# Kernel optimization log

Measured on AMD Instinct MI355X. Metric: run time of the kernel, lower is better.

The kernel has to match this reference:

```python
import jax, jax.numpy as jnp
import numpy as np

N_BINS = 50
FEATURE_ID = 0
EPS = 1e-7  # keras backend epsilon used by binary_crossentropy clipping


def setup_inputs() -> dict:
    key = jax.random.key(0)
    k1, k2 = jax.random.split(key)
    inputs = jax.random.normal(k1, (8_000_000, 4), dtype=jnp.float32)
    targets = jax.random.randint(k2, (8_000_000,), 0, 2, dtype=jnp.int32)
    return {"inputs": inputs, "targets": targets}


def _cut_forward(inputs, targets):
    # x: selected feature column, y: binary labels
    x = inputs[:, FEATURE_ID]
    y = targets
    N = x.shape[0]
    n_f = jnp.float32(N)

    x_min = jnp.min(x)
    x_max = jnp.max(x)
    E = N_BINS + 1
    edges = jnp.linspace(x_min, x_max, E)

    # Sort events once; prefix-sum of signal labels gives exact class counts
    # below/above any threshold (equivalent to the per-bin compare+count loop,
    # including the original's inclusive [lower, upper] double-counting of edges).
    order = jnp.argsort(x)
    xs = x[order]
    ys = (y[order] == 1).astype(jnp.float32)
    cs = jnp.concatenate([jnp.zeros((1,), jnp.float32), jnp.cumsum(ys)])  # [N+1]
    Ns = cs[-1]
    Nb = n_f - Ns

    r = jnp.searchsorted(xs, edges, side='right')  # count(x <= e)
    l = jnp.searchsorted(xs, edges, side='left')   # count(x <  e)
    ns_le = cs[r]
    ns_lt = cs[l]
    nb_le = r.astype(jnp.float32) - ns_le
    nb_lt = l.astype(jnp.float32) - ns_lt

    # hist[i] = count(lower[i] <= v <= upper[i]) per class
    hist0 = nb_le[1:] - nb_lt[:-1]  # background, [N_BINS]
    hist1 = ns_le[1:] - ns_lt[:-1]  # signal

    # candidate bin edges: sign-flip boundaries of hist0>hist1 with non-empty bins
    gt0 = hist0 > hist1
    cand0 = jnp.logical_xor(gt0[:-1], gt0[1:]) & (hist0[:-1] > 0)
    gt1 = hist1 > hist0
    cand1 = jnp.logical_xor(gt1[:-1], gt1[1:]) & (hist1[:-1] > 0)
    mask = jnp.zeros((E,), bool).at[1:N_BINS].set(cand0 | cand1)
    cnt = jnp.sum(mask)
    # original appends x_max when exactly one candidate survives
    mask = mask.at[-1].set(mask[-1] | (cnt == 1))

    # clipped BCE on hard 0/1 predictions reduces to a weighted error count:
    # correct sample -> -log(1-eps), wrong sample -> -log(eps)
    a = -jnp.log1p(jnp.float32(-EPS))
    b = -jnp.log(jnp.float32(EPS))

    def bce(correct):
        return ((n_f - correct) * b + correct * a) / n_f

    # per-edge losses for single-threshold cases
    c0 = ns_le + (Nb - nb_le)          # case 0: pred = (x <= c)
    c1 = (Ns - ns_lt) + nb_lt          # case 1: pred = (x >= c)
    # per-pair losses (i = lower cut, j = upper cut)
    c2 = (ns_le[None, :] - ns_lt[:, None]) + Nb - (nb_le[None, :] - nb_lt[:, None])
    c3 = ns_le[:, None] + (Ns - ns_lt[None, :]) + (nb_le[None, :] - nb_lt[:, None])

    L = jnp.stack([
        jnp.broadcast_to(bce(c0)[:, None], (E, E)),
        jnp.broadcast_to(bce(c1)[:, None], (E, E)),
        bce(c2),
        bce(c3),
    ])  # [4, E, E]
    per_pair_min = jnp.min(L, axis=0)
    per_pair_case = jnp.argmin(L, axis=0)

    idx = jnp.arange(E)
    valid = mask[:, None] & mask[None, :] & (idx[:, None] < idx[None, :])
    flat = jnp.argmin(jnp.where(valid, per_pair_min, jnp.inf))
    i = flat // E
    j = flat % E
    lower = edges[i]
    upper = edges[j]
    case = per_pair_case[i, j]

    pred0 = x <= lower
    pred1 = x >= lower
    pred2 = pred1 & (x <= upper)
    pred3 = pred0 | (x >= upper)
    y_pred = jnp.where(case == 0, pred0,
             jnp.where(case == 1, pred1,
             jnp.where(case == 2, pred2, pred3)))
    return y_pred


def reference(inputs, targets):
    return _cut_forward(inputs, targets).astype(jnp.int32)
```

## Files before the change

### kernel.cpp

```cpp
#include <hip/hip_runtime.h>
#include <math.h>
#include <stdint.h>

#define N_BINS 50
#define EDGE_N 51
#define HIST_N 52
#define NBLK 2048
#define NTHR 256

typedef unsigned int u32;
typedef unsigned short u16;
typedef unsigned char u8;


__device__ __forceinline__ float edge_at(int e, float xmin, float xmax) {
  if (e >= N_BINS) return xmax;
  float step = __fdiv_rn((float)e, (float)N_BINS);
  float omst = __fsub_rn(1.0f, step);
  return __fadd_rn(__fmul_rn(xmin, omst), __fmul_rn(xmax, step));
}

__device__ __forceinline__ float bce_f(int c, float n_f, float aC, float bC) {
  float cf = (float)c;
  float t = __fadd_rn(__fmul_rn(__fsub_rn(n_f, cf), bC), __fmul_rn(cf, aC));
  return __fdiv_rn(t, n_f);
}

__device__ __forceinline__ void get_ab(float& aC, float& bC) {
  const double epsd = (double)1e-7f;
  aC = (float)(-log1p(-epsd));
  bC = (float)(-log(epsd));
}

__device__ __forceinline__ void global_minmax(const float* __restrict__ bmin,
                                              const float* __restrict__ bmax,
                                              float* s_red, float* s_mm) {
  const int tid = threadIdx.x;
  float m = INFINITY, M = -INFINITY;
  for (int i = tid; i < NBLK; i += NTHR) { m = fminf(m, bmin[i]); M = fmaxf(M, bmax[i]); }
  for (int off = 32; off; off >>= 1) {
    m = fminf(m, __shfl_down(m, off));
    M = fmaxf(M, __shfl_down(M, off));
  }
  int wid = tid >> 6;
  if ((tid & 63) == 0) { s_red[wid] = m; s_red[4 + wid] = M; }
  __syncthreads();
  if (tid == 0) {
    float mm = s_red[0], MM = s_red[4];
    for (int w = 1; w < NTHR / 64; ++w) { mm = fminf(mm, s_red[w]); MM = fmaxf(MM, s_red[4 + w]); }
    s_mm[0] = mm;
    s_mm[1] = MM;
  }
  __syncthreads();
}

template <int COMPACT>
__global__ void k_minmax(const float4* __restrict__ in4, int n,
                         float* __restrict__ bmin, float* __restrict__ bmax,
                         int* __restrict__ histU, int* __restrict__ histE,
                         float* __restrict__ xc) {
  const int tid = threadIdx.x, bid = blockIdx.x;
  const int gid = bid * NTHR + tid;
  const int stride = NBLK * NTHR;
  const int nv = n >> 2;
  const int base = nv << 2;
  float4* __restrict__ xc4 = (float4*)xc;
  if (bid == 0) {
    for (int i = tid; i < 2 * HIST_N; i += NTHR) histU[i] = 0;
    for (int i = tid; i < 2 * EDGE_N; i += NTHR) histE[i] = 0;
  }
  float vmin = INFINITY, vmax = -INFINITY;
  for (int iv = gid; iv < nv; iv += stride) {
    float4 a = in4[4 * iv + 0];
    float4 b = in4[4 * iv + 1];
    float4 c = in4[4 * iv + 2];
    float4 d = in4[4 * iv + 3];
    vmin = fminf(fminf(vmin, fminf(a.x, b.x)), fminf(c.x, d.x));
    vmax = fmaxf(fmaxf(vmax, fmaxf(a.x, b.x)), fmaxf(c.x, d.x));
    if (COMPACT) xc4[iv] = make_float4(a.x, b.x, c.x, d.x);
  }
  if (bid == 0 && tid < (n - base)) {
    float x = in4[base + tid].x;
    vmin = fminf(vmin, x);
    vmax = fmaxf(vmax, x);
    if (COMPACT) xc[base + tid] = x;
  }
  for (int off = 32; off; off >>= 1) {
    vmin = fminf(vmin, __shfl_down(vmin, off));
    vmax = fmaxf(vmax, __shfl_down(vmax, off));
  }
  __shared__ float s_red[8];
  int wid = tid >> 6;
  if ((tid & 63) == 0) { s_red[wid] = vmin; s_red[4 + wid] = vmax; }
  __syncthreads();
  if (tid == 0) {
    float m = s_red[0], M = s_red[4];
    for (int w = 1; w < NTHR / 64; ++w) { m = fminf(m, s_red[w]); M = fmaxf(M, s_red[4 + w]); }
    bmin[bid] = m;
    bmax[bid] = M;
  }
}

template <int COMPACT>
__global__ void k_hist(const float4* __restrict__ in4, const float* __restrict__ xc,
                       const int* __restrict__ tgt, int n,
                       const float* __restrict__ bmin, const float* __restrict__ bmax,
                       int* __restrict__ histU, int* __restrict__ histE,
                       u8* __restrict__ codes) {
  __shared__ u16 ph[HIST_N][NTHR];
  __shared__ float s_edges[EDGE_N];
  __shared__ int shE[2 * EDGE_N];
  __shared__ float s_red[8];
  __shared__ float s_mm[2];
  const int tid = threadIdx.x, bid = blockIdx.x;
  global_minmax(bmin, bmax, s_red, s_mm);
  u32* ph32w = (u32*)&ph[0][0];
  for (int i = tid; i < HIST_N * (NTHR / 2); i += NTHR) ph32w[i] = 0;
  for (int i = tid; i < 2 * EDGE_N; i += NTHR) shE[i] = 0;
  const float xmin = s_mm[0], xmax = s_mm[1];
  if (tid < EDGE_N) s_edges[tid] = edge_at(tid, xmin, xmax);
  __syncthreads();
  const float delta = __fdiv_rn(__fsub_rn(xmax, xmin), (float)N_BINS);
  const float inv_delta = (delta > 0.0f) ? (1.0f / delta) : 0.0f;
  const int gid = bid * NTHR + tid;
  const int stride = NBLK * NTHR;
  const int nv = n >> 2;
  const int base = nv << 2;
  const float4* __restrict__ xc4 = (const float4*)xc;
  const int4* __restrict__ tgt4 = (const int4*)tgt;
  uchar4* __restrict__ codes4 = (uchar4*)codes;
  for (int iv = gid; iv < nv; iv += stride) {
    float xs[4];
    if (COMPACT) {
      float4 v = xc4[iv];
      xs[0] = v.x; xs[1] = v.y; xs[2] = v.z; xs[3] = v.w;
    } else {
      xs[0] = in4[4 * iv + 0].x; xs[1] = in4[4 * iv + 1].x;
      xs[2] = in4[4 * iv + 2].x; xs[3] = in4[4 * iv + 3].x;
    }
    int4 tv = tgt4[iv];
    int ts[4] = {tv.x, tv.y, tv.z, tv.w};
    u8 cd[4];
#pragma unroll
    for (int k = 0; k < 4; ++k) {
      float x = xs[k];
      int cls = (ts[k] == 1) ? 0 : 1;
      int g = (int)((x - xmin) * inv_delta);
      g = max(0, min(g, EDGE_N));
      while (g < EDGE_N && s_edges[g] < x) ++g;
      while (g > 0 && s_edges[g - 1] >= x) --g;
      int eq = (g < EDGE_N && s_edges[g] == x) ? 1 : 0;
      ph[g][tid] = (u16)(ph[g][tid] + (1u << (cls * 8)));
      if (eq) atomicAdd(&shE[cls * EDGE_N + g], 1);
      cd[k] = (u8)(g | (eq << 6));
    }
    if (COMPACT) codes4[iv] = make_uchar4(cd[0], cd[1], cd[2], cd[3]);
  }
  if (bid == 0 && tid < (n - base)) {
    int i = base + tid;
    float x = COMPACT ? xc[i] : in4[i].x;
    int cls = (tgt[i] == 1) ? 0 : 1;
    int g = (int)((x - xmin) * inv_delta);
    g = max(0, min(g, EDGE_N));
    while (g < EDGE_N && s_edges[g] < x) ++g;
    while (g > 0 && s_edges[g - 1] >= x) --g;
    int eq = (g < EDGE_N && s_edges[g] == x) ? 1 : 0;
    ph[g][tid] = (u16)(ph[g][tid] + (1u << (cls * 8)));
    if (eq) atomicAdd(&shE[cls * EDGE_N + g], 1);
    if (COMPACT) codes[i] = (u8)(g | (eq << 6));
  }
  __syncthreads();
  if (tid < HIST_N) {
    const u32* ph32r = (const u32*)&ph[0][0];
    u32 c0 = 0, c1 = 0;
    for (int k2 = 0; k2 < NTHR / 2; ++k2) {
      int idx = (k2 + tid) & (NTHR / 2 - 1);
      u32 w = ph32r[tid * (NTHR / 2) + idx];
      c0 += (w & 0xFFu) + ((w >> 16) & 0xFFu);
      c1 += ((w >> 8) & 0xFFu) + ((w >> 24) & 0xFFu);
    }
    if (c0) atomicAdd(&histU[tid], (int)c0);
    if (c1) atomicAdd(&histU[HIST_N + tid], (int)c1);
  }
  for (int kk = tid; kk < 2 * EDGE_N; kk += NTHR) {
    int v = shE[kk];
    if (v) atomicAdd(&histE[kk], v);
  }
}

template <int COMPACT>
__global__ void k_decide_pred(const float4* __restrict__ in4, const u8* __restrict__ codes,
                              int n, const float* __restrict__ bmin,
                              const float* __restrict__ bmax,
                              const int* __restrict__ histU, const int* __restrict__ histE,
                              int* __restrict__ out) {
  __shared__ float s_red[8];
  __shared__ float s_mm[2];
  __shared__ int s_ns_le[EDGE_N], s_ns_lt[EDGE_N], s_nb_le[EDGE_N], s_nb_lt[EDGE_N];
  __shared__ int s_h0[N_BINS], s_h1[N_BINS];
  __shared__ unsigned char s_g0[N_BINS], s_g1[N_BINS];
  __shared__ unsigned char s_mask[EDGE_N];
  __shared__ float s_rv[NTHR];
  __shared__ int s_ri[NTHR];
  __shared__ int s_cut[3];
  const int tid = threadIdx.x, bid = blockIdx.x;

  global_minmax(bmin, bmax, s_red, s_mm);

  if (tid < 128) {
    const int lane = tid & 63;
    const int w = tid >> 6;
    int v = (lane < EDGE_N) ? histU[w * HIST_N + lane] : 0;
#pragma unroll
    for (int d = 1; d < 64; d <<= 1) {
      int t = __shfl_up(v, d);
      if (lane >= d) v += t;
    }
    if (lane < EDGE_N) {
      int e = histE[w * EDGE_N + lane];
      if (w == 0) { s_ns_le[lane] = v; s_ns_lt[lane] = v - e; }
      else        { s_nb_le[lane] = v; s_nb_lt[lane] = v - e; }
    }
  }
  if (tid < EDGE_N) s_mask[tid] = 0;
  __syncthreads();
  if (tid < N_BINS) {
    int h0 = s_nb_le[tid + 1] - s_nb_lt[tid];
    int h1 = s_ns_le[tid + 1] - s_ns_lt[tid];
    s_h0[tid] = h0;
    s_h1[tid] = h1;
    s_g0[tid] = h0 > h1;
    s_g1[tid] = h1 > h0;
  }
  __syncthreads();
  if (tid < 64) {
    bool cand = false;
    if (tid + 1 < N_BINS) {
      bool c0 = (s_g0[tid] != s_g0[tid + 1]) && (s_h0[tid] > 0);
      bool c1 = (s_g1[tid] != s_g1[tid + 1]) && (s_h1[tid] > 0);
      cand = c0 || c1;
      if (cand) s_mask[tid + 1] = 1;
    }
    unsigned long long bal = __ballot(cand);
    if (tid == 0 && __popcll(bal) == 1) s_mask[N_BINS] = 1;
  }
  __syncthreads();
  const int Ns = s_ns_le[EDGE_N - 1];
  const int Nb = n - Ns;
  float aC, bC;
  get_ab(aC, bC);
  const float n_f = (float)n;
  float best = INFINITY;
  int bestIdx = 0x7fffffff;
  for (int p = tid; p < EDGE_N * EDGE_N; p += NTHR) {
    int i = p / EDGE_N, j = p - i * EDGE_N;
    float v = INFINITY;
    if (s_mask[i] && s_mask[j] && i < j) {
      int c0 = s_ns_le[i] + (Nb - s_nb_le[i]);
      int c1 = Ns - s_ns_lt[i] + s_nb_lt[i];
      int c2 = s_ns_le[j] - s_ns_lt[i] + Nb - (s_nb_le[j] - s_nb_lt[i]);
      int c3 = s_ns_le[i] + Ns - s_ns_lt[j] + s_nb_le[j] - s_nb_lt[i];
      float L0 = bce_f(c0, n_f, aC, bC);
      float L1 = bce_f(c1, n_f, aC, bC);
      float L2 = bce_f(c2, n_f, aC, bC);
      float L3 = bce_f(c3, n_f, aC, bC);
      v = L0;
      if (L1 < v) v = L1;
      if (L2 < v) v = L2;
      if (L3 < v) v = L3;
    }
    if (v < best || (v == best && p < bestIdx)) { best = v; bestIdx = p; }
  }
  s_rv[tid] = best;
  s_ri[tid] = bestIdx;
  __syncthreads();
  for (int s = NTHR / 2; s > 0; s >>= 1) {
    if (tid < s) {
      float ov = s_rv[tid + s];
      int oi = s_ri[tid + s];
      if (ov < s_rv[tid] || (ov == s_rv[tid] && oi < s_ri[tid])) {
        s_rv[tid] = ov;
        s_ri[tid] = oi;
      }
    }
    __syncthreads();
  }
  if (tid == 0) {
    int p = s_ri[0];
    int i = p / EDGE_N, j = p - i * EDGE_N;
    int c0 = s_ns_le[i] + (Nb - s_nb_le[i]);
    int c1 = Ns - s_ns_lt[i] + s_nb_lt[i];
    int c2 = s_ns_le[j] - s_ns_lt[i] + Nb - (s_nb_le[j] - s_nb_lt[i]);
    int c3 = s_ns_le[i] + Ns - s_ns_lt[j] + s_nb_le[j] - s_nb_lt[i];
    float L0 = bce_f(c0, n_f, aC, bC);
    float L1 = bce_f(c1, n_f, aC, bC);
    float L2 = bce_f(c2, n_f, aC, bC);
    float L3 = bce_f(c3, n_f, aC, bC);
    int cs = 0;
    float m = L0;
    if (L1 < m) { m = L1; cs = 1; }
    if (L2 < m) { m = L2; cs = 2; }
    if (L3 < m) { m = L3; cs = 3; }
    s_cut[0] = cs;
    s_cut[1] = i;
    s_cut[2] = j;
  }
  __syncthreads();

  const int cs = s_cut[0], ci = s_cut[1], cj = s_cut[2];
  const int gid = bid * NTHR + tid;
  const int stride = NBLK * NTHR;
  if (COMPACT) {
    const int4* __restrict__ c16 = (const int4*)codes;
    int4* __restrict__ out4 = (int4*)out;
    const int ncv = n >> 4;
    for (int iv = gid; iv < ncv; iv += stride) {
      int4 c = c16[iv];
      u32 wv[4] = {(u32)c.x, (u32)c.y, (u32)c.z, (u32)c.w};
#pragma unroll
      for (int q = 0; q < 4; ++q) {
        u32 w = wv[q];
        int r[4];
#pragma unroll
        for (int b = 0; b < 4; ++b) {
          u32 by = (w >> (8 * b)) & 0xFFu;
          int u = (int)(by & 63u);
          int v = u + (int)(by >> 6);
          bool p0 = (u <= ci), p1 = (ci < v);
          bool p = (cs == 0) ? p0 : (cs == 1) ? p1 : (cs == 2) ? (p1 && (u <= cj)) : (p0 || (cj < v));
          r[b] = p ? 1 : 0;
        }
        out4[iv * 4 + q] = make_int4(r[0], r[1], r[2], r[3]);
      }
    }
    const int cbase = ncv << 4;
    if (bid == 0 && tid < (n - cbase)) {
      int i = cbase + tid;
      u32 by = codes[i];
      int u = (int)(by & 63u);
      int v = u + (int)(by >> 6);
      bool p0 = (u <= ci), p1 = (ci < v);
      bool p = (cs == 0) ? p0 : (cs == 1) ? p1 : (cs == 2) ? (p1 && (u <= cj)) : (p0 || (cj < v));
      out[i] = p ? 1 : 0;
    }
  } else {
    const float xmin = s_mm[0], xmax = s_mm[1];
    const float lower = edge_at(ci, xmin, xmax);
    const float upper = edge_at(cj, xmin, xmax);
    int4* __restrict__ out4 = (int4*)out;
    const int nv = n >> 2;
    for (int iv = gid; iv < nv; iv += stride) {
      float xs[4] = {in4[4 * iv + 0].x, in4[4 * iv + 1].x, in4[4 * iv + 2].x, in4[4 * iv + 3].x};
      int r[4];
#pragma unroll
      for (int k = 0; k < 4; ++k) {
        float x = xs[k];
        bool p;
        if (cs == 0) p = (x <= lower);
        else if (cs == 1) p = (x >= lower);
        else if (cs == 2) p = (x >= lower) && (x <= upper);
        else p = (x <= lower) || (x >= upper);
        r[k] = p ? 1 : 0;
      }
      out4[iv] = make_int4(r[0], r[1], r[2], r[3]);
    }
    const int fbase = nv << 2;
    if (bid == 0 && tid < (n - fbase)) {
      int i = fbase + tid;
      float x = in4[i].x;
      bool p;
      if (cs == 0) p = (x <= lower);
      else if (cs == 1) p = (x >= lower);
      else if (cs == 2) p = (x >= lower) && (x <= upper);
      else p = (x <= lower) || (x >= upper);
      out[i] = p ? 1 : 0;
    }
  }
}

extern "C" void kernel_launch(void* const* d_in, const int* in_sizes, int n_in,
                              void* d_out, int out_size, void* d_ws, size_t ws_size,
                              hipStream_t stream) {
  const float4* in4 = (const float4*)d_in[0];
  const int* tgt = (const int*)d_in[1];
  int n = in_sizes[1];
  int* out = (int*)d_out;
  char* ws = (char*)d_ws;
  float* bmin = (float*)ws;
  float* bmax = (float*)(ws + 8192);
  int* histU = (int*)(ws + 16448);
  int* histE = histU + 2 * HIST_N;
  u8* codes = (u8*)(ws + 32768);
  size_t xcOff = ((size_t)32768 + (size_t)n + 15) & ~(size_t)15;
  float* xc = (float*)(ws + xcOff);
  const bool compact = ws_size >= xcOff + (size_t)n * 4u;

  if (compact) {
    k_minmax<1><<<NBLK, NTHR, 0, stream>>>(in4, n, bmin, bmax, histU, histE, xc);
    k_hist<1><<<NBLK, NTHR, 0, stream>>>(in4, xc, tgt, n, bmin, bmax, histU, histE, codes);
    k_decide_pred<1><<<NBLK, NTHR, 0, stream>>>(in4, codes, n, bmin, bmax, histU, histE, out);
  } else {
    k_minmax<0><<<NBLK, NTHR, 0, stream>>>(in4, n, bmin, bmax, histU, histE, nullptr);
    k_hist<0><<<NBLK, NTHR, 0, stream>>>(in4, nullptr, tgt, n, bmin, bmax, histU, histE, nullptr);
    k_decide_pred<0><<<NBLK, NTHR, 0, stream>>>(in4, nullptr, n, bmin, bmax, histU, histE, out);
  }
}
```

Before: 105.3 us.

## Widen per-thread work to 16 elements, add nontemporal loads/stores, replicate histograms

Each thread in the min/max and histogram kernels now handles 16 elements per iteration, with more loads in flight and a single 16-byte codes store. Input and target reads and output writes use nontemporal builtins to cut cache pollution on streaming data. Global histogram atomics are spread over 16 replicated copies, which the decide kernel sums, to reduce atomic contention. The wider unrolled loops raise register pressure, and nontemporal loads could hurt if the data would otherwise be reused from L2.

After: 163.5 us. +55.3%, slower.

```diff
diff --git a/kernel.cpp b/kernel.cpp
--- a/kernel.cpp
+++ b/kernel.cpp
@@ -7,10 +7,13 @@
 #define HIST_N 52
 #define NBLK 2048
 #define NTHR 256
+#define NREP 16
 
 typedef unsigned int u32;
 typedef unsigned short u16;
 typedef unsigned char u8;
+typedef float f32x4 __attribute__((ext_vector_type(4)));
+typedef int i32x4 __attribute__((ext_vector_type(4)));
 
 
 __device__ __forceinline__ float edge_at(int e, float xmin, float xmax) {
@@ -55,32 +58,39 @@
 }
 
 template <int COMPACT>
-__global__ void k_minmax(const float4* __restrict__ in4, int n,
+__global__ void k_minmax(const f32x4* __restrict__ in4, int n,
                          float* __restrict__ bmin, float* __restrict__ bmax,
-                         int* __restrict__ histU, int* __restrict__ histE,
-                         float* __restrict__ xc) {
+                         int* __restrict__ histz, float* __restrict__ xc) {
   const int tid = threadIdx.x, bid = blockIdx.x;
   const int gid = bid * NTHR + tid;
   const int stride = NBLK * NTHR;
-  const int nv = n >> 2;
-  const int base = nv << 2;
-  float4* __restrict__ xc4 = (float4*)xc;
+  const int nt16 = n >> 4;
+  const int base = nt16 << 4;
+  f32x4* __restrict__ xc4 = (f32x4*)xc;
   if (bid == 0) {
-    for (int i = tid; i < 2 * HIST_N; i += NTHR) histU[i] = 0;
-    for (int i = tid; i < 2 * EDGE_N; i += NTHR) histE[i] = 0;
+    for (int i = tid; i < NREP * (2 * HIST_N + 2 * EDGE_N); i += NTHR) histz[i] = 0;
   }
   float vmin = INFINITY, vmax = -INFINITY;
-  for (int iv = gid; iv < nv; iv += stride) {
-    float4 a = in4[4 * iv + 0];
-    float4 b = in4[4 * iv + 1];
-    float4 c = in4[4 * iv + 2];
-    float4 d = in4[4 * iv + 3];
-    vmin = fminf(fminf(vmin, fminf(a.x, b.x)), fminf(c.x, d.x));
-    vmax = fmaxf(fmaxf(vmax, fmaxf(a.x, b.x)), fmaxf(c.x, d.x));
-    if (COMPACT) xc4[iv] = make_float4(a.x, b.x, c.x, d.x);
+  for (int iv = gid; iv < nt16; iv += stride) {
+    float xs[16];
+#pragma unroll
+    for (int j = 0; j < 16; ++j) {
+      f32x4 r = __builtin_nontemporal_load(&in4[16 * iv + j]);
+      xs[j] = r.x;
+    }
+#pragma unroll
+    for (int j = 0; j < 16; ++j) { vmin = fminf(vmin, xs[j]); vmax = fmaxf(vmax, xs[j]); }
+    if (COMPACT) {
+#pragma unroll
+      for (int q = 0; q < 4; ++q) {
+        f32x4 o = {xs[4 * q], xs[4 * q + 1], xs[4 * q + 2], xs[4 * q + 3]};
+        xc4[4 * iv + q] = o;
+      }
+    }
   }
   if (bid == 0 && tid < (n - base)) {
-    float x = in4[base + tid].x;
+    f32x4 r = in4[base + tid];
+    float x = r.x;
     vmin = fminf(vmin, x);
     vmax = fmaxf(vmax, x);
     if (COMPACT) xc[base + tid] = x;
@@ -102,7 +112,7 @@
 }
 
 template <int COMPACT>
-__global__ void k_hist(const float4* __restrict__ in4, const float* __restrict__ xc,
+__global__ void k_hist(const f32x4* __restrict__ in4, const float* __restrict__ xc,
                        const int* __restrict__ tgt, int n,
                        const float* __restrict__ bmin, const float* __restrict__ bmax,
                        int* __restrict__ histU, int* __restrict__ histE,
@@ -124,25 +134,29 @@
   const float inv_delta = (delta > 0.0f) ? (1.0f / delta) : 0.0f;
   const int gid = bid * NTHR + tid;
   const int stride = NBLK * NTHR;
-  const int nv = n >> 2;
-  const int base = nv << 2;
-  const float4* __restrict__ xc4 = (const float4*)xc;
-  const int4* __restrict__ tgt4 = (const int4*)tgt;
-  uchar4* __restrict__ codes4 = (uchar4*)codes;
-  for (int iv = gid; iv < nv; iv += stride) {
-    float xs[4];
-    if (COMPACT) {
-      float4 v = xc4[iv];
-      xs[0] = v.x; xs[1] = v.y; xs[2] = v.z; xs[3] = v.w;
-    } else {
-      xs[0] = in4[4 * iv + 0].x; xs[1] = in4[4 * iv + 1].x;
-      xs[2] = in4[4 * iv + 2].x; xs[3] = in4[4 * iv + 3].x;
-    }
-    int4 tv = tgt4[iv];
-    int ts[4] = {tv.x, tv.y, tv.z, tv.w};
-    u8 cd[4];
-#pragma unroll
-    for (int k = 0; k < 4; ++k) {
+  const int nt16 = n >> 4;
+  const int base = nt16 << 4;
+  const f32x4* __restrict__ xc4 = (const f32x4*)xc;
+  const i32x4* __restrict__ tgt4 = (const i32x4*)tgt;
+  i32x4* __restrict__ codes16 = (i32x4*)codes;
+  for (int iv = gid; iv < nt16; iv += stride) {
+    float xs[16];
+    int ts[16];
+#pragma unroll
+    for (int q = 0; q < 4; ++q) {
+      f32x4 v;
+      if (COMPACT) v = xc4[4 * iv + q];
+      else {
+        v.x = in4[16 * iv + 4 * q + 0].x; v.y = in4[16 * iv + 4 * q + 1].x;
+        v.z = in4[16 * iv + 4 * q + 2].x; v.w = in4[16 * iv + 4 * q + 3].x;
+      }
+      i32x4 t = __builtin_nontemporal_load(&tgt4[4 * iv + q]);
+      xs[4 * q] = v.x; xs[4 * q + 1] = v.y; xs[4 * q + 2] = v.z; xs[4 * q + 3] = v.w;
+      ts[4 * q] = t.x; ts[4 * q + 1] = t.y; ts[4 * q + 2] = t.z; ts[4 * q + 3] = t.w;
+    }
+    u32 cw[4] = {0, 0, 0, 0};
+#pragma unroll
+    for (int k = 0; k < 16; ++k) {
       float x = xs[k];
       int cls = (ts[k] == 1) ? 0 : 1;
       int g = (int)((x - xmin) * inv_delta);
@@ -152,9 +166,12 @@
       int eq = (g < EDGE_N && s_edges[g] == x) ? 1 : 0;
       ph[g][tid] = (u16)(ph[g][tid] + (1u << (cls * 8)));
       if (eq) atomicAdd(&shE[cls * EDGE_N + g], 1);
-      cd[k] = (u8)(g | (eq << 6));
-    }
-    if (COMPACT) codes4[iv] = make_uchar4(cd[0], cd[1], cd[2], cd[3]);
+      cw[k >> 2] |= (u32)(g | (eq << 6)) << (8 * (k & 3));
+    }
+    if (COMPACT) {
+      i32x4 cv = {(int)cw[0], (int)cw[1], (int)cw[2], (int)cw[3]};
+      codes16[iv] = cv;
+    }
   }
   if (bid == 0 && tid < (n - base)) {
     int i = base + tid;
@@ -170,6 +187,8 @@
     if (COMPACT) codes[i] = (u8)(g | (eq << 6));
   }
   __syncthreads();
+  int* hU = histU + (bid & (NREP - 1)) * (2 * HIST_N);
+  int* hE = histE + (bid & (NREP - 1)) * (2 * EDGE_N);
   if (tid < HIST_N) {
     const u32* ph32r = (const u32*)&ph[0][0];
     u32 c0 = 0, c1 = 0;
@@ -179,17 +198,17 @@
       c0 += (w & 0xFFu) + ((w >> 16) & 0xFFu);
       c1 += ((w >> 8) & 0xFFu) + ((w >> 24) & 0xFFu);
     }
-    if (c0) atomicAdd(&histU[tid], (int)c0);
-    if (c1) atomicAdd(&histU[HIST_N + tid], (int)c1);
+    if (c0) atomicAdd(&hU[tid], (int)c0);
+    if (c1) atomicAdd(&hU[HIST_N + tid], (int)c1);
   }
   for (int kk = tid; kk < 2 * EDGE_N; kk += NTHR) {
     int v = shE[kk];
-    if (v) atomicAdd(&histE[kk], v);
+    if (v) atomicAdd(&hE[kk], v);
   }
 }
 
 template <int COMPACT>
-__global__ void k_decide_pred(const float4* __restrict__ in4, const u8* __restrict__ codes,
+__global__ void k_decide_pred(const f32x4* __restrict__ in4, const u8* __restrict__ codes,
                               int n, const float* __restrict__ bmin,
                               const float* __restrict__ bmax,
                               const int* __restrict__ histU, const int* __restrict__ histE,
@@ -210,14 +229,18 @@
   if (tid < 128) {
     const int lane = tid & 63;
     const int w = tid >> 6;
-    int v = (lane < EDGE_N) ? histU[w * HIST_N + lane] : 0;
+    int v = 0;
+    if (lane < EDGE_N) {
+      for (int r = 0; r < NREP; ++r) v += histU[r * (2 * HIST_N) + w * HIST_N + lane];
+    }
 #pragma unroll
     for (int d = 1; d < 64; d <<= 1) {
       int t = __shfl_up(v, d);
       if (lane >= d) v += t;
     }
     if (lane < EDGE_N) {
-      int e = histE[w * EDGE_N + lane];
+      int e = 0;
+      for (int r = 0; r < NREP; ++r) e += histE[r * (2 * EDGE_N) + w * EDGE_N + lane];
       if (w == 0) { s_ns_le[lane] = v; s_ns_lt[lane] = v - e; }
       else        { s_nb_le[lane] = v; s_nb_lt[lane] = v - e; }
     }
@@ -311,11 +334,11 @@
   const int gid = bid * NTHR + tid;
   const int stride = NBLK * NTHR;
   if (COMPACT) {
-    const int4* __restrict__ c16 = (const int4*)codes;
-    int4* __restrict__ out4 = (int4*)out;
+    const i32x4* __restrict__ c16 = (const i32x4*)codes;
+    i32x4* __restrict__ out4 = (i32x4*)out;
     const int ncv = n >> 4;
     for (int iv = gid; iv < ncv; iv += stride) {
-      int4 c = c16[iv];
+      i32x4 c = c16[iv];
       u32 wv[4] = {(u32)c.x, (u32)c.y, (u32)c.z, (u32)c.w};
 #pragma unroll
       for (int q = 0; q < 4; ++q) {
@@ -330,7 +353,8 @@
           bool p = (cs == 0) ? p0 : (cs == 1) ? p1 : (cs == 2) ? (p1 && (u <= cj)) : (p0 || (cj < v));
           r[b] = p ? 1 : 0;
         }
-        out4[iv * 4 + q] = make_int4(r[0], r[1], r[2], r[3]);
+        i32x4 ov = {r[0], r[1], r[2], r[3]};
+        __builtin_nontemporal_store(ov, &out4[iv * 4 + q]);
       }
     }
     const int cbase = ncv << 4;
@@ -347,7 +371,7 @@
     const float xmin = s_mm[0], xmax = s_mm[1];
     const float lower = edge_at(ci, xmin, xmax);
     const float upper = edge_at(cj, xmin, xmax);
-    int4* __restrict__ out4 = (int4*)out;
+    i32x4* __restrict__ out4 = (i32x4*)out;
     const int nv = n >> 2;
     for (int iv = gid; iv < nv; iv += stride) {
       float xs[4] = {in4[4 * iv + 0].x, in4[4 * iv + 1].x, in4[4 * iv + 2].x, in4[4 * iv + 3].x};
@@ -362,7 +386,8 @@
         else p = (x <= lower) || (x >= upper);
         r[k] = p ? 1 : 0;
       }
-      out4[iv] = make_int4(r[0], r[1], r[2], r[3]);
+      i32x4 ov = {r[0], r[1], r[2], r[3]};
+      __builtin_nontemporal_store(ov, &out4[iv]);
     }
     const int fbase = nv << 2;
     if (bid == 0 && tid < (n - fbase)) {
@@ -381,26 +406,26 @@
 extern "C" void kernel_launch(void* const* d_in, const int* in_sizes, int n_in,
                               void* d_out, int out_size, void* d_ws, size_t ws_size,
                               hipStream_t stream) {
-  const float4* in4 = (const float4*)d_in[0];
+  const f32x4* in4 = (const f32x4*)d_in[0];
   const int* tgt = (const int*)d_in[1];
   int n = in_sizes[1];
   int* out = (int*)d_out;
   char* ws = (char*)d_ws;
   float* bmin = (float*)ws;
   float* bmax = (float*)(ws + 8192);
-  int* histU = (int*)(ws + 16448);
-  int* histE = histU + 2 * HIST_N;
+  int* histU = (int*)(ws + 16384);
+  int* histE = (int*)(ws + 16384 + NREP * 2 * HIST_N * 4);
   u8* codes = (u8*)(ws + 32768);
   size_t xcOff = ((size_t)32768 + (size_t)n + 15) & ~(size_t)15;
   float* xc = (float*)(ws + xcOff);
   const bool compact = ws_size >= xcOff + (size_t)n * 4u;
 
   if (compact) {
-    k_minmax<1><<<NBLK, NTHR, 0, stream>>>(in4, n, bmin, bmax, histU, histE, xc);
+    k_minmax<1><<<NBLK, NTHR, 0, stream>>>(in4, n, bmin, bmax, histU, xc);
     k_hist<1><<<NBLK, NTHR, 0, stream>>>(in4, xc, tgt, n, bmin, bmax, histU, histE, codes);
     k_decide_pred<1><<<NBLK, NTHR, 0, stream>>>(in4, codes, n, bmin, bmax, histU, histE, out);
   } else {
-    k_minmax<0><<<NBLK, NTHR, 0, stream>>>(in4, n, bmin, bmax, histU, histE, nullptr);
+    k_minmax<0><<<NBLK, NTHR, 0, stream>>>(in4, n, bmin, bmax, histU, nullptr);
     k_hist<0><<<NBLK, NTHR, 0, stream>>>(in4, nullptr, tgt, n, bmin, bmax, histU, histE, nullptr);
     k_decide_pred<0><<<NBLK, NTHR, 0, stream>>>(in4, nullptr, n, bmin, bmax, histU, histE, out);
   }
```
